# Performance work log

Measured on AMD Instinct MI355X. Metric: run time of the kernel, lower is better.

Reference implementation:

```python
import jax, jax.numpy as jnp
import numpy as np

C = 256
GROUPS = 32
EPS = 1e-5


def setup_inputs() -> dict:
    key = jax.random.key(0)
    ks = jax.random.split(key, 6)
    b, c, H, W = 8, C, 64, 64
    s = 1.0 / np.sqrt(c)
    return {
        "x": jax.random.normal(ks[0], (b, c, H, W), dtype=jnp.float32),
        "gn_scale": jnp.ones((c,), jnp.float32),
        "gn_bias": jnp.zeros((c,), jnp.float32),
        "wq": jax.random.normal(ks[1], (c, c), jnp.float32) * s,
        "bq": jnp.zeros((c,), jnp.float32),
        "wk": jax.random.normal(ks[2], (c, c), jnp.float32) * s,
        "bk": jnp.zeros((c,), jnp.float32),
        "wv": jax.random.normal(ks[3], (c, c), jnp.float32) * s,
        "bv": jnp.zeros((c,), jnp.float32),
        "wo": jax.random.normal(ks[4], (c, c), jnp.float32) * s,
        "bo": jnp.zeros((c,), jnp.float32),
    }


def reference(x, gn_scale, gn_bias, wq, bq, wk, bk, wv, bv, wo, bo):
    b, c, H, W = x.shape
    N = H * W
    # GroupNorm(32, c)
    xg = x.reshape(b, GROUPS, c // GROUPS, H, W)
    mean = xg.mean(axis=(2, 3, 4), keepdims=True)
    var = xg.var(axis=(2, 3, 4), keepdims=True)
    xn = ((xg - mean) * jax.lax.rsqrt(var + EPS)).reshape(b, c, H, W)
    xn = xn * gn_scale[None, :, None, None] + gn_bias[None, :, None, None]
    xf = xn.reshape(b, c, N)  # [b, c, N]
    # 1x1 convs == per-pixel channel matmuls
    q = jnp.einsum('oc,bcn->bon', wq, xf) + bq[None, :, None]
    k = jnp.einsum('oc,bcn->bon', wk, xf) + bk[None, :, None]
    v = jnp.einsum('oc,bcn->bon', wv, xf) + bv[None, :, None]
    # attention: scores [b, N, N]
    scale = 1.0 / jnp.sqrt(jnp.asarray(c, x.dtype))
    w = jnp.einsum('bcn,bcm->bnm', q, k) * scale
    w = jax.nn.softmax(w, axis=-1)
    attn = jnp.einsum('bnm,bcm->bcn', w, v)  # [b, c, N]
    out = jnp.einsum('oc,bcn->bon', wo, attn) + bo[None, :, None]
    return x + out.reshape(b, c, H, W)
```

## Files before the change

### kernel.cpp

```cpp
#include <hip/hip_runtime.h>

typedef __attribute__((ext_vector_type(8))) short short8;
typedef __attribute__((ext_vector_type(4))) float floatx4;
typedef __attribute__((ext_vector_type(4))) int intx4;

#define NPIX 4096
#define CH 256

static __device__ __forceinline__ unsigned short f2bf(float f) {
  union { float f; unsigned int u; } v; v.f = f;
  unsigned int u = v.u;
  return (unsigned short)((u + 0x7FFFu + ((u >> 16) & 1u)) >> 16);
}

static __device__ __forceinline__ unsigned long long pack4bf(floatx4 v) {
  return (unsigned long long)f2bf(v[0]) | ((unsigned long long)f2bf(v[1]) << 16) |
         ((unsigned long long)f2bf(v[2]) << 32) | ((unsigned long long)f2bf(v[3]) << 48);
}

typedef __attribute__((address_space(3))) unsigned int lds_uint;
typedef const __attribute__((address_space(1))) unsigned int glob_uint;
static __device__ __forceinline__ void gload16(const void* g, void* l) {
  __builtin_amdgcn_global_load_lds((glob_uint*)g, (lds_uint*)l, 16, 0, 0);
}

__global__ void conv_weights_kernel(const float* __restrict__ wq, const float* __restrict__ wk,
                                    const float* __restrict__ wv, const float* __restrict__ wo,
                                    unsigned short* __restrict__ wqkv, unsigned short* __restrict__ wob) {
  int i = blockIdx.x * 256 + threadIdx.x;
  wqkv[i]          = f2bf(wq[i]);
  wqkv[65536 + i]  = f2bf(wk[i]);
  wqkv[131072 + i] = f2bf(wv[i]);
  wob[i]           = f2bf(wo[i]);
}

__global__ __launch_bounds__(256) void gn_kernel(const float* __restrict__ x,
                                                 const float* __restrict__ gsc,
                                                 const float* __restrict__ gbi,
                                                 unsigned short* __restrict__ xnT) {
  int blk = blockIdx.x; int b = blk >> 5; int g = blk & 31;
  int c0 = g * 8;
  const float* xb = x + ((size_t)b * CH + c0) * NPIX;
  int tid = threadIdx.x;
  float s = 0.f, ss = 0.f;
#pragma unroll
  for (int ci = 0; ci < 8; ++ci) {
    const floatx4* p = (const floatx4*)(xb + (size_t)ci * NPIX);
    for (int n4 = tid; n4 < 1024; n4 += 256) {
      floatx4 v = p[n4];
      s += v[0] + v[1] + v[2] + v[3];
      ss += v[0]*v[0] + v[1]*v[1] + v[2]*v[2] + v[3]*v[3];
    }
  }
#pragma unroll
  for (int o = 32; o > 0; o >>= 1) { s += __shfl_down(s, o); ss += __shfl_down(ss, o); }
  __shared__ float red[10];
  int wid = tid >> 6;
  if ((tid & 63) == 0) { red[wid] = s; red[4 + wid] = ss; }
  __syncthreads();
  if (tid == 0) {
    float S = red[0] + red[1] + red[2] + red[3];
    float SS = red[4] + red[5] + red[6] + red[7];
    float mean = S * (1.f / 32768.f);
    float var = SS * (1.f / 32768.f) - mean * mean;
    red[8] = mean; red[9] = rsqrtf(var + 1e-5f);
  }
  __syncthreads();
  float mean = red[8], rstd = red[9];
  float sc[8], bi[8];
#pragma unroll
  for (int ci = 0; ci < 8; ++ci) {
    float scale = gsc[c0 + ci] * rstd;
    sc[ci] = scale;
    bi[ci] = gbi[c0 + ci] - mean * scale;
  }
  for (int n4 = tid; n4 < 1024; n4 += 256) {
    floatx4 v[8];
#pragma unroll
    for (int ci = 0; ci < 8; ++ci) v[ci] = ((const floatx4*)(xb + (size_t)ci * NPIX))[n4];
#pragma unroll
    for (int j = 0; j < 4; ++j) {
      alignas(16) unsigned short tmp[8];
#pragma unroll
      for (int ci = 0; ci < 8; ++ci) tmp[ci] = f2bf(v[ci][j] * sc[ci] + bi[ci]);
      *(intx4*)(xnT + ((size_t)(b * NPIX + n4 * 4 + j)) * CH + c0) = *(const intx4*)tmp;
    }
  }
}

__global__ __launch_bounds__(256, 2) void qkv_gemm(
    const unsigned short* __restrict__ wqkv, const unsigned short* __restrict__ xnT,
    const float* __restrict__ bq, const float* __restrict__ bk, const float* __restrict__ bv,
    unsigned short* __restrict__ qT, unsigned short* __restrict__ kT, unsigned short* __restrict__ vC) {
  int nt = blockIdx.x, ot = blockIdx.y, bz = blockIdx.z;
  int which = bz % 3, b = bz / 3;
  const unsigned short* W = wqkv + which * 65536;
  const float* bias = which == 0 ? bq : (which == 1 ? bk : bv);
  const unsigned short* X = xnT + (size_t)b * NPIX * CH;
  int o0 = ot * 128, n0 = nt * 128;

  __shared__ unsigned short As[128 * 64];
  __shared__ unsigned short Bs[128 * 64];

  int tid = threadIdx.x;
  int wave = tid >> 6, lane = tid & 63, quad = lane >> 4, l16 = lane & 15;
  int wm = (wave >> 1) * 64, wn = (wave & 1) * 64;

  floatx4 acc[4][4];
#pragma unroll
  for (int i = 0; i < 4; ++i)
#pragma unroll
    for (int j = 0; j < 4; ++j) acc[i][j] = (floatx4){0.f, 0.f, 0.f, 0.f};

  for (int k0 = 0; k0 < 256; k0 += 64) {
    __syncthreads();
#pragma unroll
    for (int c2 = 0; c2 < 4; ++c2) {
      int row = wave * 32 + c2 * 8 + (lane >> 3);
      int sc = (lane & 7) ^ (row & 7);
      gload16(W + (size_t)(o0 + row) * CH + k0 + sc * 8, &As[(wave * 32 + c2 * 8) * 64]);
      gload16(X + (size_t)(n0 + row) * CH + k0 + sc * 8, &Bs[(wave * 32 + c2 * 8) * 64]);
    }
    __syncthreads();
#pragma unroll
    for (int s = 0; s < 2; ++s) {
      short8 af[4], bf[4];
#pragma unroll
      for (int i = 0; i < 4; ++i) {
        int m = wm + i * 16 + l16;
        af[i] = *(const short8*)(As + m * 64 + (((s * 4 + quad) ^ (m & 7)) * 8));
        int n = wn + i * 16 + l16;
        bf[i] = *(const short8*)(Bs + n * 64 + (((s * 4 + quad) ^ (n & 7)) * 8));
      }
#pragma unroll
      for (int i = 0; i < 4; ++i)
#pragma unroll
        for (int j = 0; j < 4; ++j)
          acc[i][j] = __builtin_amdgcn_mfma_f32_16x16x32_bf16(af[i], bf[j], acc[i][j], 0, 0, 0);
    }
  }

  if (which < 2) {
    float qs = (which == 0) ? 0.090168440f : 1.0f;
    unsigned short* outp = (which == 0 ? qT : kT) + (size_t)b * NPIX * CH;
#pragma unroll
    for (int i = 0; i < 4; ++i) {
      int obase = o0 + wm + i * 16 + quad * 4;
      float bias4[4];
#pragma unroll
      for (int r = 0; r < 4; ++r) bias4[r] = bias[obase + r];
#pragma unroll
      for (int j = 0; j < 4; ++j) {
        int n = n0 + wn + j * 16 + l16;
        unsigned long long pk = 0;
#pragma unroll
        for (int r = 0; r < 4; ++r)
          pk |= (unsigned long long)f2bf((acc[i][j][r] + bias4[r]) * qs) << (16 * r);
        *(unsigned long long*)(outp + (size_t)n * CH + obase) = pk;
      }
    }
  } else {
    unsigned short* outp = vC + (size_t)b * CH * NPIX;
#pragma unroll
    for (int i = 0; i < 4; ++i)
#pragma unroll
      for (int r = 0; r < 4; ++r) {
        int o = o0 + wm + i * 16 + quad * 4 + r;
        float bb = bias[o];
#pragma unroll
        for (int j = 0; j < 4; ++j) {
          int n = n0 + wn + j * 16 + l16;
          outp[(size_t)o * NPIX + n] = f2bf(acc[i][j][r] + bb);
        }
      }
  }
}

__global__ __launch_bounds__(512) void attn_kernel(
    const unsigned short* __restrict__ qT, const unsigned short* __restrict__ kT,
    const unsigned short* __restrict__ vC, unsigned short* __restrict__ aT) {
  __shared__ unsigned short Klds[2][64 * 256];
  __shared__ unsigned short Vlds[2][256 * 64];
  __shared__ unsigned short Plds[128 * 64];
  __shared__ float lred[128][2];

  const int tid = threadIdx.x;
  const int w = tid >> 6, lane = tid & 63;
  const int quad = lane >> 4, l16 = lane & 15;
  const int b = blockIdx.x & 7, qt = blockIdx.x >> 3;
  const int qbase = qt * 128;

  const unsigned short* Kb = kT + (size_t)b * NPIX * CH;
  const unsigned short* Vb = vC + (size_t)b * CH * NPIX;

  const int msl = (w & 1) * 32, qsl = (w >> 1) * 32;
  const int csl = (w & 3) * 64, qh = (w >> 2) * 64;

  short8 qf[2][8];
#pragma unroll
  for (int qsub = 0; qsub < 2; ++qsub) {
    const unsigned short* qp =
        qT + ((size_t)(b * NPIX + qbase + qsl + qsub * 16 + l16)) * CH + quad * 8;
#pragma unroll
    for (int s = 0; s < 8; ++s) qf[qsub][s] = *(const short8*)(qp + s * 32);
  }

  floatx4 oacc[4][4];
#pragma unroll
  for (int i = 0; i < 4; ++i)
#pragma unroll
    for (int j = 0; j < 4; ++j) oacc[i][j] = (floatx4){0.f, 0.f, 0.f, 0.f};
  float l_acc[2] = {0.f, 0.f};

#define STAGE(KT)                                                                         \
  {                                                                                       \
    int m0_ = (KT) * 64;                                                                  \
    int bb_ = (KT) & 1;                                                                   \
    if (w < 4) {                                                                          \
      _Pragma("unroll") for (int j = 0; j < 8; ++j) {                                     \
        int r0 = w * 16 + j * 2 + (lane >> 5);                                            \
        gload16(Kb + (size_t)(m0_ + r0) * CH + (((lane & 31) ^ (r0 & 7)) * 8),            \
                &Klds[bb_][(w * 16 + j * 2) * 256]);                                      \
      }                                                                                   \
    } else {                                                                              \
      _Pragma("unroll") for (int j = 0; j < 8; ++j) {                                     \
        int c_ = (w - 4) * 64 + j * 8 + (lane >> 3);                                      \
        gload16(Vb + (size_t)c_ * NPIX + m0_ + (((lane & 7) ^ (c_ & 7)) * 8),             \
                &Vlds[bb_][((w - 4) * 64 + j * 8) * 64]);                                 \
      }                                                                                   \
    }                                                                                     \
  }

  STAGE(0);

  for (int kt = 0; kt < 64; ++kt) {
    const int buf = kt & 1;
    asm volatile("s_waitcnt vmcnt(0) lgkmcnt(0)\ns_barrier" ::: "memory");
    if (kt + 1 < 64) STAGE(kt + 1);

    floatx4 sacc[2][2];
#pragma unroll
    for (int i = 0; i < 2; ++i)
#pragma unroll
      for (int j = 0; j < 2; ++j) sacc[i][j] = (floatx4){0.f, 0.f, 0.f, 0.f};
#pragma unroll
    for (int s = 0; s < 8; ++s) {
#pragma unroll
      for (int msub = 0; msub < 2; ++msub) {
        int m = msl + msub * 16 + l16;
        short8 kf = *(const short8*)&Klds[buf][m * 256 + (((s * 4 + quad) ^ (m & 7)) * 8)];
        sacc[msub][0] = __builtin_amdgcn_mfma_f32_16x16x32_bf16(kf, qf[0][s], sacc[msub][0], 0, 0, 0);
        sacc[msub][1] = __builtin_amdgcn_mfma_f32_16x16x32_bf16(kf, qf[1][s], sacc[msub][1], 0, 0, 0);
      }
    }
#pragma unroll
    for (int qsub = 0; qsub < 2; ++qsub) {
      float sum = 0.f;
#pragma unroll
      for (int msub = 0; msub < 2; ++msub)
#pragma unroll
        for (int r = 0; r < 4; ++r) {
          float p = exp2f(sacc[msub][qsub][r]);
          sacc[msub][qsub][r] = p; sum += p;
        }
      sum += __shfl_xor(sum, 16);
      sum += __shfl_xor(sum, 32);
      l_acc[qsub] += sum;
    }
#pragma unroll
    for (int qsub = 0; qsub < 2; ++qsub) {
      int q = qsl + qsub * 16 + l16;
#pragma unroll
      for (int msub = 0; msub < 2; ++msub) {
        int chunkm = ((msl + msub * 16) >> 3) + (quad >> 1);
        int phys = chunkm ^ (l16 & 7);
        uint2 wv;
        wv.x = (unsigned int)f2bf(sacc[msub][qsub][0]) | ((unsigned int)f2bf(sacc[msub][qsub][1]) << 16);
        wv.y = (unsigned int)f2bf(sacc[msub][qsub][2]) | ((unsigned int)f2bf(sacc[msub][qsub][3]) << 16);
        *(uint2*)&Plds[q * 64 + phys * 8 + (quad & 1) * 4] = wv;
      }
    }
    asm volatile("s_waitcnt lgkmcnt(0)\ns_barrier" ::: "memory");

#pragma unroll
    for (int mstep = 0; mstep < 2; ++mstep) {
      short8 pf[4];
#pragma unroll
      for (int qsub = 0; qsub < 4; ++qsub) {
        int q = qh + qsub * 16 + l16;
        pf[qsub] = *(const short8*)&Plds[q * 64 + (((mstep * 4 + quad) ^ (l16 & 7)) * 8)];
      }
#pragma unroll
      for (int csub = 0; csub < 4; ++csub) {
        int c = csl + csub * 16 + l16;
        short8 vf = *(const short8*)&Vlds[buf][c * 64 + (((mstep * 4 + quad) ^ (c & 7)) * 8)];
#pragma unroll
        for (int qsub = 0; qsub < 4; ++qsub)
          oacc[csub][qsub] = __builtin_amdgcn_mfma_f32_16x16x32_bf16(vf, pf[qsub], oacc[csub][qsub], 0, 0, 0);
      }
    }
  }
#undef STAGE

  if (quad == 0) {
    lred[qsl + l16][w & 1] = l_acc[0];
    lred[qsl + 16 + l16][w & 1] = l_acc[1];
  }
  __syncthreads();
  float inv[4];
#pragma unroll
  for (int qsub = 0; qsub < 4; ++qsub) {
    int q = qh + qsub * 16 + l16;
    inv[qsub] = 1.f / (lred[q][0] + lred[q][1]);
  }
  unsigned short* ab = aT + (size_t)b * NPIX * CH;
#pragma unroll
  for (int csub = 0; csub < 4; ++csub) {
    int c = csl + csub * 16 + quad * 4;
#pragma unroll
    for (int qsub = 0; qsub < 4; ++qsub) {
      int q = qbase + qh + qsub * 16 + l16;
      floatx4 o = oacc[csub][qsub];
      o[0] *= inv[qsub]; o[1] *= inv[qsub]; o[2] *= inv[qsub]; o[3] *= inv[qsub];
      *(unsigned long long*)(ab + (size_t)q * CH + c) = pack4bf(o);
    }
  }
}

__global__ __launch_bounds__(256, 2) void out_gemm(
    const unsigned short* __restrict__ wob, const unsigned short* __restrict__ aT,
    const float* __restrict__ bo, const float* __restrict__ x, float* __restrict__ outp) {
  int nt = blockIdx.x, ot = blockIdx.y, b = blockIdx.z;
  const unsigned short* A = aT + (size_t)b * NPIX * CH;
  int o0 = ot * 128, n0 = nt * 128;

  __shared__ unsigned short As[128 * 64];
  __shared__ unsigned short Bs[128 * 64];

  int tid = threadIdx.x;
  int wave = tid >> 6, lane = tid & 63, quad = lane >> 4, l16 = lane & 15;
  int wm = (wave >> 1) * 64, wn = (wave & 1) * 64;

  floatx4 acc[4][4];
#pragma unroll
  for (int i = 0; i < 4; ++i)
#pragma unroll
    for (int j = 0; j < 4; ++j) acc[i][j] = (floatx4){0.f, 0.f, 0.f, 0.f};

  for (int k0 = 0; k0 < 256; k0 += 64) {
    __syncthreads();
#pragma unroll
    for (int c2 = 0; c2 < 4; ++c2) {
      int row = wave * 32 + c2 * 8 + (lane >> 3);
      int sc = (lane & 7) ^ (row & 7);
      gload16(wob + (size_t)(o0 + row) * CH + k0 + sc * 8, &As[(wave * 32 + c2 * 8) * 64]);
      gload16(A + (size_t)(n0 + row) * CH + k0 + sc * 8, &Bs[(wave * 32 + c2 * 8) * 64]);
    }
    __syncthreads();
#pragma unroll
    for (int s = 0; s < 2; ++s) {
      short8 af[4], bf[4];
#pragma unroll
      for (int i = 0; i < 4; ++i) {
        int m = wm + i * 16 + l16;
        af[i] = *(const short8*)(As + m * 64 + (((s * 4 + quad) ^ (m & 7)) * 8));
        int n = wn + i * 16 + l16;
        bf[i] = *(const short8*)(Bs + n * 64 + (((s * 4 + quad) ^ (n & 7)) * 8));
      }
#pragma unroll
      for (int i = 0; i < 4; ++i)
#pragma unroll
        for (int j = 0; j < 4; ++j)
          acc[i][j] = __builtin_amdgcn_mfma_f32_16x16x32_bf16(af[i], bf[j], acc[i][j], 0, 0, 0);
    }
  }

#pragma unroll
  for (int i = 0; i < 4; ++i)
#pragma unroll
    for (int r = 0; r < 4; ++r) {
      int o = o0 + wm + i * 16 + quad * 4 + r;
      float bb = bo[o];
#pragma unroll
      for (int j = 0; j < 4; ++j) {
        int n = n0 + wn + j * 16 + l16;
        size_t idx = ((size_t)b * CH + o) * NPIX + n;
        outp[idx] = x[idx] + bb + acc[i][j][r];
      }
    }
}

extern "C" void kernel_launch(void* const* d_in, const int* in_sizes, int n_in,
                              void* d_out, int out_size, void* d_ws, size_t ws_size,
                              hipStream_t stream) {
  const float* x   = (const float*)d_in[0];
  const float* gsc = (const float*)d_in[1];
  const float* gbi = (const float*)d_in[2];
  const float* wq  = (const float*)d_in[3];
  const float* bq  = (const float*)d_in[4];
  const float* wk  = (const float*)d_in[5];
  const float* bk  = (const float*)d_in[6];
  const float* wv  = (const float*)d_in[7];
  const float* bv  = (const float*)d_in[8];
  const float* wo  = (const float*)d_in[9];
  const float* bo  = (const float*)d_in[10];
  float* out = (float*)d_out;

  char* ws = (char*)d_ws;
  unsigned short* xnT  = (unsigned short*)(ws);
  unsigned short* qT   = (unsigned short*)(ws + 16777216);
  unsigned short* kT   = (unsigned short*)(ws + 33554432);
  unsigned short* vC   = (unsigned short*)(ws + 50331648);
  unsigned short* wqkv = (unsigned short*)(ws + 67108864);
  unsigned short* wob  = (unsigned short*)(ws + 67502080);
  unsigned short* aT   = (unsigned short*)(ws + 67633152);

  conv_weights_kernel<<<256, 256, 0, stream>>>(wq, wk, wv, wo, wqkv, wob);
  gn_kernel<<<256, 256, 0, stream>>>(x, gsc, gbi, xnT);
  dim3 g1(32, 2, 24);
  qkv_gemm<<<g1, 256, 0, stream>>>(wqkv, xnT, bq, bk, bv, qT, kT, vC);
  attn_kernel<<<256, 512, 0, stream>>>(qT, kT, vC, aT);
  dim3 g3(32, 2, 8);
  out_gemm<<<g3, 256, 0, stream>>>(wob, aT, bo, x, out);
}
```

Measured before the change: 358.9 us.

## Switch attention MFMAs to 32x32x16 tiles, cheaper bf16 packing, two blocks per CU

Result: faster. 320.9 us (-10.6%).

```diff
diff --git a/kernel.cpp b/kernel.cpp
--- a/kernel.cpp
+++ b/kernel.cpp
@@ -2,6 +2,7 @@
 
 typedef __attribute__((ext_vector_type(8))) short short8;
 typedef __attribute__((ext_vector_type(4))) float floatx4;
+typedef __attribute__((ext_vector_type(16))) float floatx16;
 typedef __attribute__((ext_vector_type(4))) int intx4;
 
 #define NPIX 4096
@@ -13,9 +14,9 @@
   return (unsigned short)((u + 0x7FFFu + ((u >> 16) & 1u)) >> 16);
 }
 
-static __device__ __forceinline__ unsigned long long pack4bf(floatx4 v) {
-  return (unsigned long long)f2bf(v[0]) | ((unsigned long long)f2bf(v[1]) << 16) |
-         ((unsigned long long)f2bf(v[2]) << 32) | ((unsigned long long)f2bf(v[3]) << 48);
+static __device__ __forceinline__ unsigned int pk2bf(float a, float b) {
+  union { float f; unsigned int u; } x, y; x.f = a; y.f = b;
+  return __builtin_amdgcn_perm(y.u + 0x8000u, x.u + 0x8000u, 0x07060302u);
 }
 
 typedef __attribute__((address_space(3))) unsigned int lds_uint;
@@ -152,11 +153,10 @@
 #pragma unroll
       for (int j = 0; j < 4; ++j) {
         int n = n0 + wn + j * 16 + l16;
-        unsigned long long pk = 0;
-#pragma unroll
-        for (int r = 0; r < 4; ++r)
-          pk |= (unsigned long long)f2bf((acc[i][j][r] + bias4[r]) * qs) << (16 * r);
-        *(unsigned long long*)(outp + (size_t)n * CH + obase) = pk;
+        uint2 pk;
+        pk.x = pk2bf((acc[i][j][0] + bias4[0]) * qs, (acc[i][j][1] + bias4[1]) * qs);
+        pk.y = pk2bf((acc[i][j][2] + bias4[2]) * qs, (acc[i][j][3] + bias4[3]) * qs);
+        *(uint2*)(outp + (size_t)n * CH + obase) = pk;
       }
     }
   } else {
@@ -176,7 +176,7 @@
   }
 }
 
-__global__ __launch_bounds__(512) void attn_kernel(
+__global__ __launch_bounds__(512, 2) void attn_kernel(
     const unsigned short* __restrict__ qT, const unsigned short* __restrict__ kT,
     const unsigned short* __restrict__ vC, unsigned short* __restrict__ aT) {
   __shared__ unsigned short Klds[2][64 * 256];
@@ -186,7 +186,7 @@
 
   const int tid = threadIdx.x;
   const int w = tid >> 6, lane = tid & 63;
-  const int quad = lane >> 4, l16 = lane & 15;
+  const int l32 = lane & 31, h = lane >> 5;
   const int b = blockIdx.x & 7, qt = blockIdx.x >> 3;
   const int qbase = qt * 128;
 
@@ -196,21 +196,15 @@
   const int msl = (w & 1) * 32, qsl = (w >> 1) * 32;
   const int csl = (w & 3) * 64, qh = (w >> 2) * 64;
 
-  short8 qf[2][8];
-#pragma unroll
-  for (int qsub = 0; qsub < 2; ++qsub) {
-    const unsigned short* qp =
-        qT + ((size_t)(b * NPIX + qbase + qsl + qsub * 16 + l16)) * CH + quad * 8;
-#pragma unroll
-    for (int s = 0; s < 8; ++s) qf[qsub][s] = *(const short8*)(qp + s * 32);
-  }
-
-  floatx4 oacc[4][4];
-#pragma unroll
-  for (int i = 0; i < 4; ++i)
-#pragma unroll
-    for (int j = 0; j < 4; ++j) oacc[i][j] = (floatx4){0.f, 0.f, 0.f, 0.f};
-  float l_acc[2] = {0.f, 0.f};
+  short8 qf[16];
+  {
+    const unsigned short* qp = qT + ((size_t)(b * NPIX + qbase + qsl + l32)) * CH + h * 8;
+#pragma unroll
+    for (int s = 0; s < 16; ++s) qf[s] = *(const short8*)(qp + s * 16);
+  }
+
+  floatx16 oacc[2][2] = {};
+  float l_acc = 0.f;
 
 #define STAGE(KT)                                                                         \
   {                                                                                       \
@@ -238,93 +232,86 @@
     asm volatile("s_waitcnt vmcnt(0) lgkmcnt(0)\ns_barrier" ::: "memory");
     if (kt + 1 < 64) STAGE(kt + 1);
 
-    floatx4 sacc[2][2];
-#pragma unroll
-    for (int i = 0; i < 2; ++i)
-#pragma unroll
-      for (int j = 0; j < 2; ++j) sacc[i][j] = (floatx4){0.f, 0.f, 0.f, 0.f};
-#pragma unroll
-    for (int s = 0; s < 8; ++s) {
-#pragma unroll
-      for (int msub = 0; msub < 2; ++msub) {
-        int m = msl + msub * 16 + l16;
-        short8 kf = *(const short8*)&Klds[buf][m * 256 + (((s * 4 + quad) ^ (m & 7)) * 8)];
-        sacc[msub][0] = __builtin_amdgcn_mfma_f32_16x16x32_bf16(kf, qf[0][s], sacc[msub][0], 0, 0, 0);
-        sacc[msub][1] = __builtin_amdgcn_mfma_f32_16x16x32_bf16(kf, qf[1][s], sacc[msub][1], 0, 0, 0);
-      }
-    }
+    floatx16 sacc = {};
+    {
+      const int m = msl + l32;
+      const unsigned short* kr = &Klds[buf][m * 256];
+      const int mx = m & 7;
+#pragma unroll
+      for (int s = 0; s < 16; ++s) {
+        short8 kf = *(const short8*)(kr + (((s * 2 + h) ^ mx) * 8));
+        sacc = __builtin_amdgcn_mfma_f32_32x32x16_bf16(kf, qf[s], sacc, 0, 0, 0);
+      }
+    }
+    float sum = 0.f;
+#pragma unroll
+    for (int r = 0; r < 16; ++r) {
+      float p = exp2f(sacc[r]);
+      sacc[r] = p; sum += p;
+    }
+    sum += __shfl_xor(sum, 32);
+    l_acc += sum;
+
+    {
+      int qrow = qsl + l32;
+#pragma unroll
+      for (int t = 0; t < 4; ++t) {
+        int phys = ((msl >> 3) + t) ^ (qrow & 7);
+        uint2 wv;
+        wv.x = pk2bf(sacc[4 * t], sacc[4 * t + 1]);
+        wv.y = pk2bf(sacc[4 * t + 2], sacc[4 * t + 3]);
+        *(uint2*)&Plds[qrow * 64 + phys * 8 + h * 4] = wv;
+      }
+    }
+    asm volatile("s_waitcnt lgkmcnt(0)\ns_barrier" ::: "memory");
+
+#pragma unroll
+    for (int mstep = 0; mstep < 4; ++mstep) {
+      short8 pf[2], vf[2];
+#pragma unroll
+      for (int qsub = 0; qsub < 2; ++qsub) {
+        int q = qh + qsub * 32 + l32;
+        pf[qsub] = *(const short8*)&Plds[q * 64 + (((mstep * 2 + h) ^ (q & 7)) * 8)];
+      }
+#pragma unroll
+      for (int csub = 0; csub < 2; ++csub) {
+        int c = csl + csub * 32 + l32;
+        vf[csub] = *(const short8*)&Vlds[buf][c * 64 + (((mstep * 2 + h) ^ (c & 7)) * 8)];
+      }
+#pragma unroll
+      for (int csub = 0; csub < 2; ++csub)
+#pragma unroll
+        for (int qsub = 0; qsub < 2; ++qsub)
+          oacc[csub][qsub] =
+              __builtin_amdgcn_mfma_f32_32x32x16_bf16(vf[csub], pf[qsub], oacc[csub][qsub], 0, 0, 0);
+    }
+  }
+#undef STAGE
+
+  if (lane < 32) lred[qsl + l32][w & 1] = l_acc;
+  __syncthreads();
+  float inv[2];
+#pragma unroll
+  for (int qsub = 0; qsub < 2; ++qsub) {
+    int q = qh + qsub * 32 + l32;
+    inv[qsub] = 1.f / (lred[q][0] + lred[q][1]);
+  }
+  unsigned short* ab = aT + (size_t)b * NPIX * CH;
+#pragma unroll
+  for (int csub = 0; csub < 2; ++csub)
 #pragma unroll
     for (int qsub = 0; qsub < 2; ++qsub) {
-      float sum = 0.f;
-#pragma unroll
-      for (int msub = 0; msub < 2; ++msub)
-#pragma unroll
-        for (int r = 0; r < 4; ++r) {
-          float p = exp2f(sacc[msub][qsub][r]);
-          sacc[msub][qsub][r] = p; sum += p;
-        }
-      sum += __shfl_xor(sum, 16);
-      sum += __shfl_xor(sum, 32);
-      l_acc[qsub] += sum;
-    }
-#pragma unroll
-    for (int qsub = 0; qsub < 2; ++qsub) {
-      int q = qsl + qsub * 16 + l16;
-#pragma unroll
-      for (int msub = 0; msub < 2; ++msub) {
-        int chunkm = ((msl + msub * 16) >> 3) + (quad >> 1);
-        int phys = chunkm ^ (l16 & 7);
+      int qg = qbase + qh + qsub * 32 + l32;
+      float iv = inv[qsub];
+#pragma unroll
+      for (int t = 0; t < 4; ++t) {
+        int c = csl + csub * 32 + 8 * t + 4 * h;
         uint2 wv;
-        wv.x = (unsigned int)f2bf(sacc[msub][qsub][0]) | ((unsigned int)f2bf(sacc[msub][qsub][1]) << 16);
-        wv.y = (unsigned int)f2bf(sacc[msub][qsub][2]) | ((unsigned int)f2bf(sacc[msub][qsub][3]) << 16);
-        *(uint2*)&Plds[q * 64 + phys * 8 + (quad & 1) * 4] = wv;
-      }
-    }
-    asm volatile("s_waitcnt lgkmcnt(0)\ns_barrier" ::: "memory");
-
-#pragma unroll
-    for (int mstep = 0; mstep < 2; ++mstep) {
-      short8 pf[4];
-#pragma unroll
-      for (int qsub = 0; qsub < 4; ++qsub) {
-        int q = qh + qsub * 16 + l16;
-        pf[qsub] = *(const short8*)&Plds[q * 64 + (((mstep * 4 + quad) ^ (l16 & 7)) * 8)];
-      }
-#pragma unroll
-      for (int csub = 0; csub < 4; ++csub) {
-        int c = csl + csub * 16 + l16;
-        short8 vf = *(const short8*)&Vlds[buf][c * 64 + (((mstep * 4 + quad) ^ (c & 7)) * 8)];
-#pragma unroll
-        for (int qsub = 0; qsub < 4; ++qsub)
-          oacc[csub][qsub] = __builtin_amdgcn_mfma_f32_16x16x32_bf16(vf, pf[qsub], oacc[csub][qsub], 0, 0, 0);
-      }
-    }
-  }
-#undef STAGE
-
-  if (quad == 0) {
-    lred[qsl + l16][w & 1] = l_acc[0];
-    lred[qsl + 16 + l16][w & 1] = l_acc[1];
-  }
-  __syncthreads();
-  float inv[4];
-#pragma unroll
-  for (int qsub = 0; qsub < 4; ++qsub) {
-    int q = qh + qsub * 16 + l16;
-    inv[qsub] = 1.f / (lred[q][0] + lred[q][1]);
-  }
-  unsigned short* ab = aT + (size_t)b * NPIX * CH;
-#pragma unroll
-  for (int csub = 0; csub < 4; ++csub) {
-    int c = csl + csub * 16 + quad * 4;
-#pragma unroll
-    for (int qsub = 0; qsub < 4; ++qsub) {
-      int q = qbase + qh + qsub * 16 + l16;
-      floatx4 o = oacc[csub][qsub];
-      o[0] *= inv[qsub]; o[1] *= inv[qsub]; o[2] *= inv[qsub]; o[3] *= inv[qsub];
-      *(unsigned long long*)(ab + (size_t)q * CH + c) = pack4bf(o);
-    }
-  }
+        wv.x = pk2bf(oacc[csub][qsub][4 * t] * iv, oacc[csub][qsub][4 * t + 1] * iv);
+        wv.y = pk2bf(oacc[csub][qsub][4 * t + 2] * iv, oacc[csub][qsub][4 * t + 3] * iv);
+        *(uint2*)(ab + (size_t)qg * CH + c) = wv;
+      }
+    }
 }
 
 __global__ __launch_bounds__(256, 2) void out_gemm(
```
